# Kernel tuning notes

Hardware: AMD Instinct MI355X
Metric: run time of the kernel (lower is better)

Reference implementation:

```python
import jax, jax.numpy as jnp
import numpy as np
import math

N, H, V, K = 8192, 1024, 50257, 4096

def setup_inputs() -> dict:
    key = jax.random.key(0)
    k_in, k_tgt, k_noise, k_w, k_up = jax.random.split(key, 5)
    inp = jax.random.normal(k_in, (N, H), dtype=jnp.float32)
    target = jax.random.randint(k_tgt, (N,), 0, V)
    noise = jax.random.randint(k_noise, (K,), 0, V)  # alias-multinomial draw, fixed here
    stdv = 1.0 / math.sqrt(H)
    weight = jax.random.uniform(k_w, (V, H), dtype=jnp.float32, minval=-stdv, maxval=stdv)
    bias = jnp.full((V,), -math.log(V), dtype=jnp.float32)
    up = jax.random.uniform(k_up, (V,), dtype=jnp.float32, minval=1e-6, maxval=1.0)
    unigram_prob = up / jnp.sum(up)
    return {"input": inp, "weight": weight, "bias": bias,
            "unigram_prob": unigram_prob, "target": target, "noise": noise}

def reference(input, weight, bias, unigram_prob, target, noise):
    # 'train' mode of linear_nce
    w_target = weight[target]                      # [N, H] gather
    b_target = bias[target]                        # [N]
    pmt = jnp.exp(jnp.sum(input * w_target, axis=1) + b_target)   # [N]
    pnt = unigram_prob[target]                     # [N]
    w_noise = weight[noise]                        # [K, H] gather
    b_noise = bias[noise]                          # [K]
    pmn = jnp.exp(jnp.einsum('nh,kh->nk', input, w_noise) + b_noise)  # [N, K]
    pnn = jnp.broadcast_to(unigram_prob[noise][None, :], (input.shape[0], noise.shape[0]))  # [N, K]
    return (pmt, pnt, pmn, pnn)
```

## Files before the change

kernel.cpp:

```cpp
#include <hip/hip_runtime.h>
#include <hip/hip_bf16.h>

#define NROWS 8192
#define HDIM  1024
#define VDIM  50257
#define KNOISE 4096

typedef short  bf16x8 __attribute__((ext_vector_type(8)));
typedef float  f32x4  __attribute__((ext_vector_type(4)));

__device__ __forceinline__ unsigned short f2bf(float x) {
    union { float f; unsigned int u; } v; v.f = x;
    unsigned int r = (v.u + 0x7fffu + ((v.u >> 16) & 1u)) >> 16;
    return (unsigned short)r;
}

__device__ __forceinline__ void gload16(const void* g, void* l) {
    __builtin_amdgcn_global_load_lds(
        (const __attribute__((address_space(1))) void*)g,
        (__attribute__((address_space(3))) void*)l, 16, 0, 0);
}

__global__ __launch_bounds__(256) void prep_kernel(
        const float* __restrict__ input,
        const float* __restrict__ weight,
        const float* __restrict__ bias,
        const float* __restrict__ unigram,
        const int* __restrict__ target,
        const int* __restrict__ noise,
        unsigned short* __restrict__ in_bf,
        unsigned short* __restrict__ wn_bf,
        float* __restrict__ bn,
        float* __restrict__ un,
        float* __restrict__ out_pmt,
        float* __restrict__ out_pnt) {
    const int tid = threadIdx.x;
    if (blockIdx.x < NROWS) {
        const int row = blockIdx.x;
        const int t = target[row];
        float4 a = ((const float4*)(input + (size_t)row * HDIM))[tid];
        ushort4 o;
        o.x = f2bf(a.x); o.y = f2bf(a.y); o.z = f2bf(a.z); o.w = f2bf(a.w);
        ((ushort4*)(in_bf + (size_t)row * HDIM))[tid] = o;
        float4 w = ((const float4*)(weight + (size_t)t * HDIM))[tid];
        float s = a.x * w.x + a.y * w.y + a.z * w.z + a.w * w.w;
        #pragma unroll
        for (int off = 32; off > 0; off >>= 1) s += __shfl_down(s, off);
        __shared__ float red[4];
        if ((tid & 63) == 0) red[tid >> 6] = s;
        __syncthreads();
        if (tid == 0) {
            float tot = red[0] + red[1] + red[2] + red[3];
            out_pmt[row] = expf(tot + bias[t]);
            out_pnt[row] = unigram[t];
        }
    } else {
        const int r = blockIdx.x - NROWS;
        const int idx = noise[r];
        float4 v = ((const float4*)(weight + (size_t)idx * HDIM))[tid];
        ushort4 o;
        o.x = f2bf(v.x); o.y = f2bf(v.y); o.z = f2bf(v.z); o.w = f2bf(v.w);
        ((ushort4*)(wn_bf + (size_t)r * HDIM))[tid] = o;
        if (tid == 0) { bn[r] = bias[idx]; un[r] = unigram[idx]; }
    }
}

#define BM 128
#define BN 128
#define EPS_LD 68
#define EPS_WAVE (16 * EPS_LD)
#define SMEM_BYTES 32768

__global__ __launch_bounds__(256) void gemm_nce_kernel(
        const unsigned short* __restrict__ A,
        const unsigned short* __restrict__ Bt,
        const float* __restrict__ bn,
        const float* __restrict__ un,
        float* __restrict__ pmn,
        float* __restrict__ pnn) {
    __shared__ char smem[SMEM_BYTES];
    unsigned short* As = (unsigned short*)smem;
    unsigned short* Bs = (unsigned short*)(smem + 16384);

    const int tid  = threadIdx.x;
    const int lane = tid & 63;
    const int wave = tid >> 6;
    const int wm = wave & 1;
    const int wn = wave >> 1;
    const int row0 = blockIdx.x * BM;
    const int col0 = blockIdx.y * BN;

    const int r = lane & 15;
    const int q = lane >> 4;

    f32x4 acc[4][4];
    #pragma unroll
    for (int mi = 0; mi < 4; mi++)
        #pragma unroll
        for (int ni = 0; ni < 4; ni++)
            acc[mi][ni] = (f32x4){0.f, 0.f, 0.f, 0.f};

    const int ch0 = wave * 2;
    const int ch1 = wave * 2 + 1;
    const int lr = lane >> 2;
    const int lc = (lane & 3) * 8;
    const unsigned short* aT = A  + (size_t)row0 * HDIM;
    const unsigned short* bT = Bt + (size_t)col0 * HDIM;
    const unsigned short* ga0 = aT + (size_t)(ch0 * 16 + lr) * HDIM + lc;
    const unsigned short* ga1 = aT + (size_t)(ch1 * 16 + lr) * HDIM + lc;
    const unsigned short* gb0 = bT + (size_t)(ch0 * 16 + lr) * HDIM + lc;
    const unsigned short* gb1 = bT + (size_t)(ch1 * 16 + lr) * HDIM + lc;

    const int rrd = lane >> 4;
    const int crd = (lane & 15) * 4;
    const float4 unv4 = *(const float4*)&un[col0 + wn * 64 + crd];
    float* pnn_base = pnn + (size_t)(row0 + wm * 64) * KNOISE + col0 + wn * 64 + crd;

    for (int k0 = 0; k0 < HDIM; k0 += 64) {
        gload16(ga0 + k0,      &As[ch0 * 512]);
        gload16(ga1 + k0,      &As[ch1 * 512]);
        gload16(ga0 + k0 + 32, &As[4096 + ch0 * 512]);
        gload16(ga1 + k0 + 32, &As[4096 + ch1 * 512]);
        gload16(gb0 + k0,      &Bs[ch0 * 512]);
        gload16(gb1 + k0,      &Bs[ch1 * 512]);
        gload16(gb0 + k0 + 32, &Bs[4096 + ch0 * 512]);
        gload16(gb1 + k0 + 32, &Bs[4096 + ch1 * 512]);
        __syncthreads();

        #pragma unroll
        for (int p = 0; p < 2; p++) {
            bf16x8 af[4], bfr[4];
            #pragma unroll
            for (int mi = 0; mi < 4; mi++)
                af[mi] = *(const bf16x8*)(&As[p * 4096 + (wm * 64 + mi * 16 + r) * 32 + q * 8]);
            #pragma unroll
            for (int ni = 0; ni < 4; ni++)
                bfr[ni] = *(const bf16x8*)(&Bs[p * 4096 + (wn * 64 + ni * 16 + r) * 32 + q * 8]);
            #pragma unroll
            for (int mi = 0; mi < 4; mi++)
                #pragma unroll
                for (int ni = 0; ni < 4; ni++)
                    acc[mi][ni] = __builtin_amdgcn_mfma_f32_16x16x32_bf16(af[mi], bfr[ni], acc[mi][ni], 0, 0, 0);
        }

        {
            int t = k0 >> 6;
            *(float4*)&pnn_base[(size_t)(rrd + 4 * t) * KNOISE] = unv4;
        }
        __syncthreads();
    }

    float* eps = (float*)smem + wave * EPS_WAVE;

    float bnv[4];
    #pragma unroll
    for (int ni = 0; ni < 4; ni++)
        bnv[ni] = bn[col0 + wn * 64 + ni * 16 + r];

    #pragma unroll
    for (int mi = 0; mi < 4; mi++) {
        #pragma unroll
        for (int ni = 0; ni < 4; ni++)
            #pragma unroll
            for (int j = 0; j < 4; j++)
                eps[(q * 4 + j) * EPS_LD + ni * 16 + r] = __expf(acc[mi][ni][j] + bnv[ni]);
        __builtin_amdgcn_s_waitcnt(0xc07f);
        #pragma unroll
        for (int j = 0; j < 4; j++) {
            float4 v = *(float4*)&eps[(rrd * 4 + j) * EPS_LD + crd];
            size_t off = (size_t)(row0 + wm * 64 + mi * 16 + rrd * 4 + j) * KNOISE
                       + col0 + wn * 64 + crd;
            *(float4*)&pmn[off] = v;
        }
        __builtin_amdgcn_s_waitcnt(0xc07f);
    }
}

extern "C" void kernel_launch(void* const* d_in, const int* in_sizes, int n_in,
                              void* d_out, int out_size, void* d_ws, size_t ws_size,
                              hipStream_t stream) {
    const float* input   = (const float*)d_in[0];
    const float* weight  = (const float*)d_in[1];
    const float* bias    = (const float*)d_in[2];
    const float* unigram = (const float*)d_in[3];
    const int*   target  = (const int*)d_in[4];
    const int*   noise   = (const int*)d_in[5];

    unsigned short* in_bf = (unsigned short*)d_ws;
    unsigned short* wn_bf = in_bf + (size_t)NROWS * HDIM;
    float* bn = (float*)(wn_bf + (size_t)KNOISE * HDIM);
    float* un = bn + KNOISE;

    float* out = (float*)d_out;
    float* o_pmt = out;
    float* o_pnt = out + NROWS;
    float* o_pmn = out + 2 * NROWS;
    float* o_pnn = o_pmn + (size_t)NROWS * KNOISE;

    prep_kernel<<<NROWS + KNOISE, 256, 0, stream>>>(
        input, weight, bias, unigram, target, noise,
        in_bf, wn_bf, bn, un, o_pmt, o_pnt);

    dim3 grid(NROWS / BM, KNOISE / BN);
    gemm_nce_kernel<<<grid, 256, 0, stream>>>(in_bf, wn_bf, bn, un, o_pmn, o_pnn);
}
```

Before: 469.2 us.

## Rewrite GEMM as 256x256 tiled, multi-stage LDS ring pipeline with swizzle

Replaces the 128x128 single-buffered GEMM with 256x256 tiles on 512-thread blocks, staging A and B half-tiles into a 5-slot LDS ring with async global-to-LDS loads issued ahead of compute. LDS uses an XOR swizzle to avoid bank conflicts, block IDs are remapped for L2 locality, and MFMA sections get raised priority. The goal is to hide load latency and raise reuse per byte loaded, at the cost of 160KB dynamic LDS, which forces one block per CU despite launch_bounds(512,2), plus more complex waitcnt/barrier logic.

```diff
diff --git a/kernel.cpp b/kernel.cpp
--- a/kernel.cpp
+++ b/kernel.cpp
@@ -65,111 +65,150 @@
     }
 }
 
-#define BM 128
-#define BN 128
+#define BM 256
+#define BN 256
+#define ASLOT 16384
+#define BRING_OFF 81920
 #define EPS_LD 68
-#define EPS_WAVE (16 * EPS_LD)
-#define SMEM_BYTES 32768
-
-__global__ __launch_bounds__(256) void gemm_nce_kernel(
+#define SMEM_DYN 163840
+
+__global__ __launch_bounds__(512, 2) void gemm_nce_kernel(
         const unsigned short* __restrict__ A,
         const unsigned short* __restrict__ Bt,
         const float* __restrict__ bn,
         const float* __restrict__ un,
         float* __restrict__ pmn,
         float* __restrict__ pnn) {
-    __shared__ char smem[SMEM_BYTES];
-    unsigned short* As = (unsigned short*)smem;
-    unsigned short* Bs = (unsigned short*)(smem + 16384);
+    extern __shared__ char smem[];
 
     const int tid  = threadIdx.x;
+    const int wave = tid >> 6;
     const int lane = tid & 63;
-    const int wave = tid >> 6;
-    const int wm = wave & 1;
-    const int wn = wave >> 1;
-    const int row0 = blockIdx.x * BM;
-    const int col0 = blockIdx.y * BN;
-
-    const int r = lane & 15;
-    const int q = lane >> 4;
-
-    f32x4 acc[4][4];
-    #pragma unroll
-    for (int mi = 0; mi < 4; mi++)
-        #pragma unroll
-        for (int ni = 0; ni < 4; ni++)
-            acc[mi][ni] = (f32x4){0.f, 0.f, 0.f, 0.f};
-
-    const int ch0 = wave * 2;
-    const int ch1 = wave * 2 + 1;
-    const int lr = lane >> 2;
-    const int lc = (lane & 3) * 8;
-    const unsigned short* aT = A  + (size_t)row0 * HDIM;
-    const unsigned short* bT = Bt + (size_t)col0 * HDIM;
-    const unsigned short* ga0 = aT + (size_t)(ch0 * 16 + lr) * HDIM + lc;
-    const unsigned short* ga1 = aT + (size_t)(ch1 * 16 + lr) * HDIM + lc;
-    const unsigned short* gb0 = bT + (size_t)(ch0 * 16 + lr) * HDIM + lc;
-    const unsigned short* gb1 = bT + (size_t)(ch1 * 16 + lr) * HDIM + lc;
-
-    const int rrd = lane >> 4;
-    const int crd = (lane & 15) * 4;
-    const float4 unv4 = *(const float4*)&un[col0 + wn * 64 + crd];
-    float* pnn_base = pnn + (size_t)(row0 + wm * 64) * KNOISE + col0 + wn * 64 + crd;
-
-    for (int k0 = 0; k0 < HDIM; k0 += 64) {
-        gload16(ga0 + k0,      &As[ch0 * 512]);
-        gload16(ga1 + k0,      &As[ch1 * 512]);
-        gload16(ga0 + k0 + 32, &As[4096 + ch0 * 512]);
-        gload16(ga1 + k0 + 32, &As[4096 + ch1 * 512]);
-        gload16(gb0 + k0,      &Bs[ch0 * 512]);
-        gload16(gb1 + k0,      &Bs[ch1 * 512]);
-        gload16(gb0 + k0 + 32, &Bs[4096 + ch0 * 512]);
-        gload16(gb1 + k0 + 32, &Bs[4096 + ch1 * 512]);
-        __syncthreads();
-
-        #pragma unroll
-        for (int p = 0; p < 2; p++) {
-            bf16x8 af[4], bfr[4];
-            #pragma unroll
-            for (int mi = 0; mi < 4; mi++)
-                af[mi] = *(const bf16x8*)(&As[p * 4096 + (wm * 64 + mi * 16 + r) * 32 + q * 8]);
-            #pragma unroll
-            for (int ni = 0; ni < 4; ni++)
-                bfr[ni] = *(const bf16x8*)(&Bs[p * 4096 + (wn * 64 + ni * 16 + r) * 32 + q * 8]);
-            #pragma unroll
-            for (int mi = 0; mi < 4; mi++)
-                #pragma unroll
-                for (int ni = 0; ni < 4; ni++)
-                    acc[mi][ni] = __builtin_amdgcn_mfma_f32_16x16x32_bf16(af[mi], bfr[ni], acc[mi][ni], 0, 0, 0);
-        }
-
-        {
-            int t = k0 >> 6;
-            *(float4*)&pnn_base[(size_t)(rrd + 4 * t) * KNOISE] = unv4;
-        }
-        __syncthreads();
-    }
-
-    float* eps = (float*)smem + wave * EPS_WAVE;
-
+    const int wm   = wave >> 2;
+    const int wn2  = wave & 3;
+    const int r    = lane & 15;
+    const int q    = lane >> 4;
+    const int swz  = (r & 7) << 4;
+
+    const int bid  = blockIdx.x;
+    const int swzb = (bid & 7) * 64 + (bid >> 3);
+    const int row0 = (swzb & 31) * BM;
+    const int col0 = (swzb >> 5) * BN;
+
+    const int lrow   = tid >> 3;
+    const int lchunk = tid & 7;
+    const int lsc    = lchunk ^ (lrow & 7);
+    const unsigned short* gA = A  + (size_t)(row0 + lrow) * HDIM + lsc * 8;
+    const unsigned short* gB = Bt + (size_t)(col0 + lrow) * HDIM + lsc * 8;
+    char* ldsAw = smem + wave * 1024;
+    char* ldsBw = smem + BRING_OFF + wave * 1024;
+
+    auto stageA = [&](int h) {
+        const unsigned short* g = gA + (size_t)((h & 1) * 128) * HDIM + (h >> 1) * 64;
+        char* l = ldsAw + (h % 5) * ASLOT;
+        gload16(g, l);
+        gload16(g + 64 * HDIM, l + 8192);
+    };
+    auto stageB = [&](int h) {
+        const unsigned short* g = gB + (size_t)((h & 1) * 128) * HDIM + (h >> 1) * 64;
+        char* l = ldsBw + (h % 5) * ASLOT;
+        gload16(g, l);
+        gload16(g + 64 * HDIM, l + 8192);
+    };
+
+    const int rrd = q;
+    const int crd = r * 4;
+    const float4 unv4 = *(const float4*)&un[col0 + wn2 * 64 + crd];
     float bnv[4];
     #pragma unroll
     for (int ni = 0; ni < 4; ni++)
-        bnv[ni] = bn[col0 + wn * 64 + ni * 16 + r];
-
+        bnv[ni] = bn[col0 + wn2 * 64 + ni * 16 + r];
+    float* pnn_base = pnn + (size_t)(row0 + wm * 128 + rrd) * KNOISE
+                          + col0 + wn2 * 64 + crd;
+
+    f32x4 acc[8][4];
     #pragma unroll
-    for (int mi = 0; mi < 4; mi++) {
+    for (int mi = 0; mi < 8; mi++)
         #pragma unroll
         for (int ni = 0; ni < 4; ni++)
-            #pragma unroll
-            for (int j = 0; j < 4; j++)
+            acc[mi][ni] = (f32x4){0.f, 0.f, 0.f, 0.f};
+
+    stageA(0); stageB(0); stageA(1); stageB(1); stageA(2); stageB(2);
+    asm volatile("s_waitcnt vmcnt(4)" ::: "memory");
+    __builtin_amdgcn_s_barrier();
+
+    int slotA = wm;
+    int slotB = wn2 >> 1;
+    const int koff0 = (q * 16) ^ swz;
+    const int koff1 = (64 + q * 16) ^ swz;
+
+    for (int t = 0; t < 16; ++t) {
+        const char* As = smem + slotA * ASLOT;
+        const char* Bs = smem + BRING_OFF + slotB * ASLOT;
+        #pragma unroll
+        for (int p = 0; p < 4; ++p) {
+            const int mih = p >> 1, nih = p & 1;
+            bf16x8 af[4][2], bv[2][2];
+            #pragma unroll
+            for (int m4 = 0; m4 < 4; ++m4) {
+                const int rb = (mih * 64 + m4 * 16 + r) << 7;
+                af[m4][0] = *(const bf16x8*)(As + rb + koff0);
+                af[m4][1] = *(const bf16x8*)(As + rb + koff1);
+            }
+            #pragma unroll
+            for (int n2 = 0; n2 < 2; ++n2) {
+                const int cb = ((wn2 & 1) * 64 + nih * 32 + n2 * 16 + r) << 7;
+                bv[n2][0] = *(const bf16x8*)(Bs + cb + koff0);
+                bv[n2][1] = *(const bf16x8*)(Bs + cb + koff1);
+            }
+            if (p == 0)      { if (t <= 14) stageA(2 * t + 3); }
+            else if (p == 1) { if (t <= 14) stageB(2 * t + 3); }
+            else if (p == 2) {
+                float* pb = pnn_base + (size_t)(8 * t) * KNOISE;
+                *(float4*)pb = unv4;
+                *(float4*)(pb + 4 * KNOISE) = unv4;
+                if (t <= 13) stageA(2 * t + 4);
+            } else           { if (t <= 13) stageB(2 * t + 4); }
+
+            __builtin_amdgcn_s_barrier();
+            asm volatile("s_waitcnt lgkmcnt(0)" ::: "memory");
+            __builtin_amdgcn_sched_barrier(0);
+            __builtin_amdgcn_s_setprio(1);
+            #pragma unroll
+            for (int m4 = 0; m4 < 4; ++m4)
+                #pragma unroll
+                for (int n2 = 0; n2 < 2; ++n2) {
+                    f32x4 c = acc[mih * 4 + m4][nih * 2 + n2];
+                    c = __builtin_amdgcn_mfma_f32_16x16x32_bf16(af[m4][0], bv[n2][0], c, 0, 0, 0);
+                    c = __builtin_amdgcn_mfma_f32_16x16x32_bf16(af[m4][1], bv[n2][1], c, 0, 0, 0);
+                    acc[mih * 4 + m4][nih * 2 + n2] = c;
+                }
+            __builtin_amdgcn_s_setprio(0);
+            __builtin_amdgcn_sched_barrier(0);
+            if (p == 3) {
+                if (t < 14)       { asm volatile("s_waitcnt vmcnt(6)" ::: "memory"); }
+                else if (t == 14) { asm volatile("s_waitcnt vmcnt(2)" ::: "memory"); }
+            }
+            __builtin_amdgcn_s_barrier();
+        }
+        slotA += 2; if (slotA >= 5) slotA -= 5;
+        slotB += 2; if (slotB >= 5) slotB -= 5;
+    }
+
+    float* eps = (float*)smem + wave * (16 * EPS_LD);
+    #pragma unroll
+    for (int mi = 0; mi < 8; ++mi) {
+        #pragma unroll
+        for (int ni = 0; ni < 4; ++ni)
+            #pragma unroll
+            for (int j = 0; j < 4; ++j)
                 eps[(q * 4 + j) * EPS_LD + ni * 16 + r] = __expf(acc[mi][ni][j] + bnv[ni]);
         __builtin_amdgcn_s_waitcnt(0xc07f);
         #pragma unroll
-        for (int j = 0; j < 4; j++) {
+        for (int j = 0; j < 4; ++j) {
             float4 v = *(float4*)&eps[(rrd * 4 + j) * EPS_LD + crd];
-            size_t off = (size_t)(row0 + wm * 64 + mi * 16 + rrd * 4 + j) * KNOISE
-                       + col0 + wn * 64 + crd;
+            size_t off = (size_t)(row0 + wm * 128 + mi * 16 + rrd * 4 + j) * KNOISE
+                       + col0 + wn2 * 64 + crd;
             *(float4*)&pmn[off] = v;
         }
         __builtin_amdgcn_s_waitcnt(0xc07f);
@@ -197,10 +236,18 @@
     float* o_pmn = out + 2 * NROWS;
     float* o_pnn = o_pmn + (size_t)NROWS * KNOISE;
 
+    static bool attr_done = false;
+    if (!attr_done) {
+        (void)hipFuncSetAttribute(reinterpret_cast<const void*>(gemm_nce_kernel),
+                                  hipFuncAttributeMaxDynamicSharedMemorySize,
+                                  SMEM_DYN);
+        attr_done = true;
+    }
+
     prep_kernel<<<NROWS + KNOISE, 256, 0, stream>>>(
         input, weight, bias, unigram, target, noise,
         in_bf, wn_bf, bn, un, o_pmt, o_pnt);
 
-    dim3 grid(NROWS / BM, KNOISE / BN);
-    gemm_nce_kernel<<<grid, 256, 0, stream>>>(in_bf, wn_bf, bn, un, o_pmn, o_pnn);
-}
+    gemm_nce_kernel<<<512, 512, SMEM_DYN, stream>>>(
+        in_bf, wn_bf, bn, un, o_pmn, o_pnn);
+}
```

Measured after the change: 447.6 us. 4.6% less time.
